# Optimization experiments

Hardware: AMD Instinct MI355X
Metric: run time of the kernel (lower is better)

The kernel has to match this reference:

```python
import jax, jax.numpy as jnp
import numpy as np

ELEM_ID = 3.0  # mocked pw element id for 'agentLemming'
B, C, H, W = 16, 20, 512, 512


def _step(world, fall_left):
    # torch.roll semantics: get_above = roll(+1, H-axis), get_below = roll(-1, H-axis),
    # get_left = roll(+1, W-axis), get_right = roll(-1, W-axis)
    shift_w = 1 if fall_left else -1
    density = world[:, 1:2]                                   # [B,1,H,W]
    is_element = world[:, 0:1] == ELEM_ID                     # pw.get_bool(world,'agentLemming')
    density_forward = jnp.roll(density, shift_w, axis=3)
    density_above = jnp.roll(density, 1, axis=2)
    density_forward_above = jnp.roll(density_above, shift_w, axis=3)
    does_become_above = (is_element
                         & (density_forward - density >= 0)
                         & (density_above - density < 0)
                         & (density_forward_above - density < 0))
    does_become_below = jnp.roll(does_become_above, -1, axis=2)
    world_above = jnp.roll(world, 1, axis=2)
    world_below = jnp.roll(world, -1, axis=2)
    a = does_become_above.astype(world.dtype)                 # broadcasts [B,1,H,W] over C
    b = does_become_below.astype(world.dtype)
    # interp2: (~a & ~b)*if_false + a*if_a + b*if_b  (sums if both switches fire, as in torch)
    return (1.0 - a) * (1.0 - b) * world + a * world_above + b * world_below


def setup_inputs() -> dict:
    key = jax.random.key(0)
    k1, k2, k3, k4, k5 = jax.random.split(key, 5)
    world = jax.random.normal(k1, (B, C, H, W), dtype=jnp.float32)
    # channel 0 holds integer element ids; id 3 == agentLemming
    elem_ids = jax.random.randint(k5, (B, 1, H, W), 0, 10).astype(jnp.float32)
    world = world.at[:, 0:1].set(elem_ids)
    rand_movement = jax.random.uniform(k2, (B, 1, H, W), dtype=jnp.float32)
    rand_interact = jax.random.uniform(k3, (B, 1, H, W), dtype=jnp.float32)
    rand_element = jax.random.uniform(k4, (B, 1, H, W), dtype=jnp.float32)
    return {"world": world, "rand_movement": rand_movement,
            "rand_interact": rand_interact, "rand_element": rand_element}


def reference(world, rand_movement, rand_interact, rand_element):
    # rand_* are unpacked from info but unused by BehaviorLemming
    world = _step(world, fall_left=True)
    world = _step(world, fall_left=False)
    return world
```

## Files before the change

kernel.cpp:

```cpp
#include <hip/hip_runtime.h>

#define Bn 16
#define Cn 20
#define Hn 512
#define Wn 512
#define HWn (Hn*Wn)

__device__ unsigned char g_a1[(size_t)Bn*HWn];
__device__ unsigned char g_a2[(size_t)Bn*HWn];

__global__ __launch_bounds__(256) void mask1_kernel(const float* __restrict__ world) {
    int idx = blockIdx.x * 256 + threadIdx.x;
    int w = idx & (Wn - 1);
    int h = (idx >> 9) & (Hn - 1);
    int b = idx >> 18;
    const float* e = world + (size_t)b * Cn * HWn;
    const float* d = e + HWn;
    int wm = (w - 1) & (Wn - 1);
    int hm = (h - 1) & (Hn - 1);
    float dc  = d[h  * Wn + w];
    float df  = d[h  * Wn + wm];
    float da  = d[hm * Wn + w];
    float dfa = d[hm * Wn + wm];
    bool a = (e[h * Wn + w] == 3.0f) & (df - dc >= 0.0f) & (da - dc < 0.0f) & (dfa - dc < 0.0f);
    g_a1[idx] = (unsigned char)a;
}

__device__ __forceinline__ float stepval(const float* __restrict__ p,
                                         const unsigned char* __restrict__ a1p,
                                         int r, int wc) {
    int rm = (r - 1) & (Hn - 1), rp = (r + 1) & (Hn - 1);
    unsigned char a  = a1p[r  * Wn + wc];
    unsigned char bb = a1p[rp * Wn + wc];
    float v;
    if (a)       { v = p[rm * Wn + wc]; if (bb) v += p[rp * Wn + wc]; }
    else if (bb) { v = p[rp * Wn + wc]; }
    else         { v = p[r  * Wn + wc]; }
    return v;
}

__global__ __launch_bounds__(256) void mask2_kernel(const float* __restrict__ world) {
    int idx = blockIdx.x * 256 + threadIdx.x;
    int w = idx & (Wn - 1);
    int h = (idx >> 9) & (Hn - 1);
    int b = idx >> 18;
    const float* e = world + (size_t)b * Cn * HWn;
    const float* d = e + HWn;
    const unsigned char* a1p = g_a1 + (size_t)b * HWn;
    int wp = (w + 1) & (Wn - 1);
    int hm = (h - 1) & (Hn - 1);
    float I0   = stepval(e, a1p, h,  w);
    float I1c  = stepval(d, a1p, h,  w);
    float I1f  = stepval(d, a1p, h,  wp);
    float I1a  = stepval(d, a1p, hm, w);
    float I1fa = stepval(d, a1p, hm, wp);
    bool a = (I0 == 3.0f) & (I1f - I1c >= 0.0f) & (I1a - I1c < 0.0f) & (I1fa - I1c < 0.0f);
    g_a2[idx] = (unsigned char)a;
}

__global__ __launch_bounds__(256) void final_kernel(const float* __restrict__ world,
                                                    float* __restrict__ out) {
    int idx = blockIdx.x * 256 + threadIdx.x;
    int wq = idx & (Wn / 4 - 1);
    int h  = (idx >> 7) & (Hn - 1);
    int b  = idx >> 16;
    int w  = wq * 4;

    const unsigned char* a1p = g_a1 + (size_t)b * HWn;
    const unsigned char* a2p = g_a2 + (size_t)b * HWn;
    int hm2 = (h - 2) & (Hn - 1), hm1 = (h - 1) & (Hn - 1);
    int hp1 = (h + 1) & (Hn - 1), hp2 = (h + 2) & (Hn - 1);

    float cm2[4], cm1[4], c0[4], cp1[4], cp2[4];
#pragma unroll
    for (int j = 0; j < 4; j++) {
        int wc = w + j;
        float r_m1 = (float)a1p[hm1 * Wn + wc];
        float r_0  = (float)a1p[h   * Wn + wc];
        float r_p1 = (float)a1p[hp1 * Wn + wc];
        float r_p2 = (float)a1p[hp2 * Wn + wc];
        float s0 = (float)a2p[h   * Wn + wc];
        float s1 = (float)a2p[hp1 * Wn + wc];
        float A2m = s0, A2p = s1, A2z = (1.f - s0) * (1.f - s1);
        cm2[j] = A2m * r_m1;
        cm1[j] = A2m * (1.f - r_m1) * (1.f - r_0) + A2z * r_0;
        c0[j]  = A2m * r_0 + A2z * (1.f - r_0) * (1.f - r_p1) + A2p * r_p1;
        cp1[j] = A2z * r_p1 + A2p * (1.f - r_p1) * (1.f - r_p2);
        cp2[j] = A2p * r_p2;
    }

    const float* base  = world + (size_t)b * Cn * HWn;
    float*       obase = out   + (size_t)b * Cn * HWn;
#pragma unroll 4
    for (int c = 0; c < Cn; c++) {
        const float* p = base + (size_t)c * HWn;
        float4 x_m2 = *(const float4*)(p + hm2 * Wn + w);
        float4 x_m1 = *(const float4*)(p + hm1 * Wn + w);
        float4 x_0  = *(const float4*)(p + h   * Wn + w);
        float4 x_p1 = *(const float4*)(p + hp1 * Wn + w);
        float4 x_p2 = *(const float4*)(p + hp2 * Wn + w);
        float4 r;
        r.x = cm2[0]*x_m2.x + cm1[0]*x_m1.x + c0[0]*x_0.x + cp1[0]*x_p1.x + cp2[0]*x_p2.x;
        r.y = cm2[1]*x_m2.y + cm1[1]*x_m1.y + c0[1]*x_0.y + cp1[1]*x_p1.y + cp2[1]*x_p2.y;
        r.z = cm2[2]*x_m2.z + cm1[2]*x_m1.z + c0[2]*x_0.z + cp1[2]*x_p1.z + cp2[2]*x_p2.z;
        r.w = cm2[3]*x_m2.w + cm1[3]*x_m1.w + c0[3]*x_0.w + cp1[3]*x_p1.w + cp2[3]*x_p2.w;
        *(float4*)(obase + (size_t)c * HWn + h * Wn + w) = r;
    }
}

extern "C" void kernel_launch(void* const* d_in, const int* in_sizes, int n_in,
                              void* d_out, int out_size, void* d_ws, size_t ws_size,
                              hipStream_t stream) {
    const float* world = (const float*)d_in[0];
    float* out = (float*)d_out;

    mask1_kernel<<<(Bn * HWn) / 256, 256, 0, stream>>>(world);
    mask2_kernel<<<(Bn * HWn) / 256, 256, 0, stream>>>(world);
    final_kernel<<<(Bn * Hn * (Wn / 4)) / 256, 256, 0, stream>>>(world, out);
}
```

Baseline: 693.6 us.

## Tile final kernel over row strips with sliding window and packed masks

The final kernel now gives each thread a strip of 16 rows and a group of 5 channels, not one row across all 20 channels. Rows are kept in a register sliding window, so each input row is loaded about once rather than five times. The per-pixel masks are read as packed 4-byte words and combined with bitwise logic into packed coefficient bits. Outputs use nontemporal stores. In exchange it launches fewer threads, which may lower parallelism and occupancy, and the loop is serial per thread.

```diff
diff --git a/kernel.cpp b/kernel.cpp
--- a/kernel.cpp
+++ b/kernel.cpp
@@ -5,6 +5,11 @@
 #define Hn 512
 #define Wn 512
 #define HWn (Hn*Wn)
+#define Rn 16
+#define CGn 4
+#define CPG 5
+
+typedef float f32x4 __attribute__((ext_vector_type(4)));
 
 __device__ unsigned char g_a1[(size_t)Bn*HWn];
 __device__ unsigned char g_a2[(size_t)Bn*HWn];
@@ -60,51 +65,75 @@
 
 __global__ __launch_bounds__(256) void final_kernel(const float* __restrict__ world,
                                                     float* __restrict__ out) {
-    int idx = blockIdx.x * 256 + threadIdx.x;
-    int wq = idx & (Wn / 4 - 1);
-    int h  = (idx >> 7) & (Hn - 1);
-    int b  = idx >> 16;
-    int w  = wq * 4;
+    int t    = blockIdx.x * 256 + threadIdx.x;
+    int wq   = t & 127;
+    int cg   = (t >> 7) & 3;
+    int tile = (t >> 9) & 31;
+    int b    = t >> 14;
+    int w    = wq * 4;
+    int h0   = tile * Rn;
 
     const unsigned char* a1p = g_a1 + (size_t)b * HWn;
     const unsigned char* a2p = g_a2 + (size_t)b * HWn;
-    int hm2 = (h - 2) & (Hn - 1), hm1 = (h - 1) & (Hn - 1);
-    int hp1 = (h + 1) & (Hn - 1), hp2 = (h + 2) & (Hn - 1);
 
-    float cm2[4], cm1[4], c0[4], cp1[4], cp2[4];
+    unsigned int a1r[Rn + 3];
+    unsigned int a2r[Rn + 1];
 #pragma unroll
-    for (int j = 0; j < 4; j++) {
-        int wc = w + j;
-        float r_m1 = (float)a1p[hm1 * Wn + wc];
-        float r_0  = (float)a1p[h   * Wn + wc];
-        float r_p1 = (float)a1p[hp1 * Wn + wc];
-        float r_p2 = (float)a1p[hp2 * Wn + wc];
-        float s0 = (float)a2p[h   * Wn + wc];
-        float s1 = (float)a2p[hp1 * Wn + wc];
-        float A2m = s0, A2p = s1, A2z = (1.f - s0) * (1.f - s1);
-        cm2[j] = A2m * r_m1;
-        cm1[j] = A2m * (1.f - r_m1) * (1.f - r_0) + A2z * r_0;
-        c0[j]  = A2m * r_0 + A2z * (1.f - r_0) * (1.f - r_p1) + A2p * r_p1;
-        cp1[j] = A2z * r_p1 + A2p * (1.f - r_p1) * (1.f - r_p2);
-        cp2[j] = A2p * r_p2;
+    for (int r = 0; r < Rn + 3; r++) {
+        int h = (h0 - 1 + r) & (Hn - 1);
+        a1r[r] = *(const unsigned int*)(a1p + (size_t)h * Wn + w);
+    }
+#pragma unroll
+    for (int r = 0; r < Rn + 1; r++) {
+        int h = (h0 + r) & (Hn - 1);
+        a2r[r] = *(const unsigned int*)(a2p + (size_t)h * Wn + w);
     }
 
-    const float* base  = world + (size_t)b * Cn * HWn;
-    float*       obase = out   + (size_t)b * Cn * HWn;
-#pragma unroll 4
-    for (int c = 0; c < Cn; c++) {
-        const float* p = base + (size_t)c * HWn;
-        float4 x_m2 = *(const float4*)(p + hm2 * Wn + w);
-        float4 x_m1 = *(const float4*)(p + hm1 * Wn + w);
-        float4 x_0  = *(const float4*)(p + h   * Wn + w);
-        float4 x_p1 = *(const float4*)(p + hp1 * Wn + w);
-        float4 x_p2 = *(const float4*)(p + hp2 * Wn + w);
-        float4 r;
-        r.x = cm2[0]*x_m2.x + cm1[0]*x_m1.x + c0[0]*x_0.x + cp1[0]*x_p1.x + cp2[0]*x_p2.x;
-        r.y = cm2[1]*x_m2.y + cm1[1]*x_m1.y + c0[1]*x_0.y + cp1[1]*x_p1.y + cp2[1]*x_p2.y;
-        r.z = cm2[2]*x_m2.z + cm1[2]*x_m1.z + c0[2]*x_0.z + cp1[2]*x_p1.z + cp2[2]*x_p2.z;
-        r.w = cm2[3]*x_m2.w + cm1[3]*x_m1.w + c0[3]*x_0.w + cp1[3]*x_p1.w + cp2[3]*x_p2.w;
-        *(float4*)(obase + (size_t)c * HWn + h * Wn + w) = r;
+    const unsigned int ONE = 0x01010101u;
+    unsigned int cw[Rn];
+#pragma unroll
+    for (int r = 0; r < Rn; r++) {
+        unsigned int rm1 = a1r[r], r0 = a1r[r + 1], rp1 = a1r[r + 2], rp2 = a1r[r + 3];
+        unsigned int s0 = a2r[r], s1 = a2r[r + 1];
+        unsigned int z   = (s0 | s1) ^ ONE;
+        unsigned int cm2 = s0 & rm1;
+        unsigned int cm1 = (s0 & (rm1 ^ ONE) & (r0 ^ ONE)) | (z & r0);
+        unsigned int c0  = (s0 & r0) + (z & (r0 ^ ONE) & (rp1 ^ ONE)) + (s1 & rp1);
+        unsigned int cp1 = (z & rp1) | (s1 & (rp1 ^ ONE) & (rp2 ^ ONE));
+        unsigned int cp2 = s1 & rp2;
+        cw[r] = cm2 | (cm1 << 1) | ((c0 & ONE) << 2) | (((c0 >> 1) & ONE) << 3)
+                    | (cp1 << 4) | (cp2 << 5);
+    }
+
+    const float* base  = world + ((size_t)b * Cn + (size_t)cg * CPG) * HWn + w;
+    float*       obase = out   + ((size_t)b * Cn + (size_t)cg * CPG) * HWn + w;
+
+#pragma unroll 1
+    for (int c = 0; c < CPG; c++) {
+        const float* p = base  + (size_t)c * HWn;
+        float*       q = obase + (size_t)c * HWn;
+        f32x4 xm2 = *(const f32x4*)(p + (size_t)((h0 - 2) & (Hn - 1)) * Wn);
+        f32x4 xm1 = *(const f32x4*)(p + (size_t)((h0 - 1) & (Hn - 1)) * Wn);
+        f32x4 x0  = *(const f32x4*)(p + (size_t)h0 * Wn);
+        f32x4 xp1 = *(const f32x4*)(p + (size_t)(h0 + 1) * Wn);
+#pragma unroll
+        for (int r = 0; r < Rn; r++) {
+            f32x4 xp2 = *(const f32x4*)(p + (size_t)((h0 + r + 2) & (Hn - 1)) * Wn);
+            unsigned int cwr = cw[r];
+            f32x4 o;
+#pragma unroll
+            for (int j = 0; j < 4; j++) {
+                unsigned int u = (cwr >> (8 * j)) & 0xffu;
+                float fm2 = (float)(u & 1u);
+                float fm1 = (float)((u >> 1) & 1u);
+                float f0  = (float)((u >> 2) & 3u);
+                float fp1 = (float)((u >> 4) & 1u);
+                float fp2 = (float)((u >> 5) & 1u);
+                o[j] = fm2 * xm2[j] + fm1 * xm1[j] + f0 * x0[j] + fp1 * xp1[j] + fp2 * xp2[j];
+            }
+            __builtin_nontemporal_store(o, (f32x4*)(q + (size_t)(h0 + r) * Wn));
+            xm2 = xm1; xm1 = x0; x0 = xp1; xp1 = xp2;
+        }
     }
 }
 
@@ -116,5 +145,5 @@
 
     mask1_kernel<<<(Bn * HWn) / 256, 256, 0, stream>>>(world);
     mask2_kernel<<<(Bn * HWn) / 256, 256, 0, stream>>>(world);
-    final_kernel<<<(Bn * Hn * (Wn / 4)) / 256, 256, 0, stream>>>(world, out);
+    final_kernel<<<(Bn * (Hn / Rn) * CGn * (Wn / 4)) / 256, 256, 0, stream>>>(world, out);
 }
```

Result: faster. 647.8 us (-6.6%).
